# Performance work log

Hardware: AMD Instinct MI355X
Metric: run time of the kernel (lower is better)

The kernel has to match this reference:

```python
import math
import jax, jax.numpy as jnp
import numpy as np
from jax import lax

FEATURE_DIM = 1024
EMBED_DIM = 300
VOCAB = 32000
HIDDEN = 512
BATCH = 64
MAX_LEN = 40
S = 3  # number of feature maps summed in l_total


def setup_inputs() -> dict:
    key = jax.random.key(0)
    ks = jax.random.split(key, 10)
    l_total = jax.random.normal(ks[0], (S, BATCH, FEATURE_DIM), jnp.float32)
    encoded_captions = jax.random.randint(ks[1], (BATCH, MAX_LEN), 0, VOCAB)
    lengths = jax.random.randint(ks[2], (BATCH,), 5, MAX_LEN + 1)
    lengths = lengths.at[0].set(MAX_LEN)  # ensure max(decode_lengths) == MAX_LEN-1 (static)
    caption_lengths = lengths[:, None]
    # parameters (per PlainDecoder.init_weights / torch defaults)
    emb_weight = jax.random.uniform(ks[3], (VOCAB, EMBED_DIM), jnp.float32, -0.1, 0.1)
    k = 1.0 / math.sqrt(HIDDEN)
    W_ih = jax.random.uniform(ks[4], (4 * HIDDEN, EMBED_DIM + FEATURE_DIM), jnp.float32, -k, k)
    W_hh = jax.random.uniform(ks[5], (4 * HIDDEN, HIDDEN), jnp.float32, -k, k)
    b_ih = jax.random.uniform(ks[6], (4 * HIDDEN,), jnp.float32, -k, k)
    b_hh = jax.random.uniform(ks[7], (4 * HIDDEN,), jnp.float32, -k, k)
    wdc_W = jax.random.uniform(ks[8], (VOCAB, HIDDEN), jnp.float32, -0.1, 0.1)
    wdc_b = jnp.zeros((VOCAB,), jnp.float32)
    return {
        "l_total": l_total,
        "encoded_captions": encoded_captions,
        "caption_lengths": caption_lengths,
        "emb_weight": emb_weight,
        "W_ih": W_ih,
        "W_hh": W_hh,
        "b_ih": b_ih,
        "b_hh": b_hh,
        "wdc_W": wdc_W,
        "wdc_b": wdc_b,
    }


def reference(l_total, encoded_captions, caption_lengths, emb_weight, W_ih, W_hh, b_ih, b_hh, wdc_W, wdc_b):
    # l_total: (S, B, F) -> permute(1,2,0).sum(-1) -> (B, F)
    lt = jnp.transpose(l_total, (1, 2, 0)).sum(-1)
    lengths = caption_lengths[:, 0]
    sort_ind = jnp.argsort(-lengths)  # descending
    lengths_s = lengths[sort_ind]
    lt = lt[sort_ind]
    caps = encoded_captions[sort_ind]
    decode_lengths = lengths_s - 1
    embeds = emb_weight[caps]  # (B, L, E)

    T = caps.shape[1] - 1  # static max decode length (max length pinned in setup)
    B = caps.shape[0]
    H = W_hh.shape[1]

    emb_seq = jnp.transpose(embeds[:, :T, :], (1, 0, 2))  # (T, B, E)
    mask = jnp.arange(T)[:, None] < decode_lengths[None, :]  # (T, B)

    def step(carry, xs):
        h, c = carry
        emb_t, mask_t = xs
        x = jnp.concatenate([emb_t, lt], axis=1)  # (B, E+F)
        gates = x @ W_ih.T + h @ W_hh.T + b_ih + b_hh  # (B, 4H)
        i, f, g, o = jnp.split(gates, 4, axis=1)  # torch gate order: i,f,g,o
        i = jax.nn.sigmoid(i)
        f = jax.nn.sigmoid(f)
        g = jnp.tanh(g)
        o = jax.nn.sigmoid(o)
        c = f * c + i * g
        h = o * jnp.tanh(c)
        pred = h @ wdc_W.T + wdc_b  # (B, V)
        pred = jnp.where(mask_t[:, None], pred, jnp.zeros((), pred.dtype))
        return (h, c), pred

    h0 = jnp.zeros((B, H), lt.dtype)
    c0 = jnp.zeros((B, H), lt.dtype)
    _, preds = lax.scan(step, (h0, c0), (emb_seq, mask))  # (T, B, V)
    predictions = jnp.transpose(preds, (1, 0, 2))  # (B, T, V)
    return predictions, caps, decode_lengths, sort_ind
```

## Files before the change

### kernel.cpp

```cpp
#include <hip/hip_runtime.h>
#include <hip/hip_bf16.h>
#include <math.h>

typedef float f32x4 __attribute__((ext_vector_type(4)));
typedef __bf16 bf16x8 __attribute__((ext_vector_type(8)));
typedef __bf16 bf16x4 __attribute__((ext_vector_type(4)));
typedef unsigned long long u64;

#define BATCH   64
#define TSTEPS  39
#define HID     512
#define GATES   2048
#define NVOCAB  32000
#define EMBD    300
#define FEAT    1024
#define XDIM    1324

#define PRED_ELEMS (BATCH*TSTEPS*NVOCAB)

#define WS_CNT     0
#define WS_SORT    256
#define WS_DECLEN  512
#define WS_CAPS    1024
#define WS_BAR     16384
#define WS_LT      65536
#define WS_CONST   327680
#define WS_XP      1048576
#define WS_HALL    22020096
#define WS_WDCB    25165824

__device__ __forceinline__ u64 agent_load_u64(const u64* p) {
    return __hip_atomic_load(p, __ATOMIC_RELAXED, __HIP_MEMORY_SCOPE_AGENT);
}
__device__ __forceinline__ unsigned int agent_load_u32(const unsigned int* p) {
    return __hip_atomic_load(p, __ATOMIC_RELAXED, __HIP_MEMORY_SCOPE_AGENT);
}
__device__ __forceinline__ void agent_store_u32(unsigned int* p, unsigned int v) {
    __hip_atomic_store(p, v, __ATOMIC_RELAXED, __HIP_MEMORY_SCOPE_AGENT);
}

__global__ void k0_setup(const int* caplen, const int* enc,
                         float* out_caps, float* out_declen, float* out_sort,
                         int* ws_sort, int* ws_declen, int* ws_caps,
                         unsigned int* bar) {
    __shared__ int L[BATCH];
    __shared__ int sind[BATCH];
    int tid = threadIdx.x;
    for (int x = tid; x < 64*32; x += blockDim.x) bar[x] = 0u;
    if (tid < BATCH) L[tid] = caplen[tid];
    __syncthreads();
    if (tid < BATCH) {
        int len = L[tid];
        int rank = 0;
        for (int j = 0; j < BATCH; ++j) {
            int lj = L[j];
            if (lj > len || (lj == len && j < tid)) rank++;
        }
        sind[rank] = tid;
    }
    __syncthreads();
    if (tid < BATCH) {
        int src = sind[tid];
        ws_sort[tid] = src;
        int dl = L[src] - 1;
        ws_declen[tid] = dl;
        out_declen[tid] = (float)dl;
        out_sort[tid] = (float)src;
    }
    __syncthreads();
    for (int x = tid; x < BATCH*40; x += blockDim.x) {
        int b = x / 40, t = x % 40;
        int v = enc[sind[b]*40 + t];
        ws_caps[x] = v;
        out_caps[x] = (float)v;
    }
}

__global__ void k1_lt(const float* l_total, const int* ws_sort, float* lt) {
    int b = blockIdx.x;
    int ob = ws_sort[b];
    for (int k4 = threadIdx.x; k4 < FEAT/4; k4 += blockDim.x) {
        float4 a = ((const float4*)(l_total + (0*BATCH + ob)*FEAT))[k4];
        float4 c = ((const float4*)(l_total + (1*BATCH + ob)*FEAT))[k4];
        float4 d = ((const float4*)(l_total + (2*BATCH + ob)*FEAT))[k4];
        float4 r;
        r.x = a.x + c.x + d.x;  r.y = a.y + c.y + d.y;
        r.z = a.z + c.z + d.z;  r.w = a.w + c.w + d.w;
        ((float4*)(lt + b*FEAT))[k4] = r;
    }
}

__global__ void k2_const(const float* W_ih, const float* lt,
                         const float* b_ih, const float* b_hh, float* cst) {
    __shared__ float As[32][68];
    __shared__ float Bs[32][36];
    int ctile = blockIdx.x;
    int btile = blockIdx.y;
    int tid = threadIdx.x;
    int ty = tid >> 4, tx = tid & 15;
    float acc[4][2] = {};
    for (int kc = 0; kc < 32; ++kc) {
        __syncthreads();
        #pragma unroll
        for (int j = 0; j < 8; ++j) {
            int idx = tid + j*256;
            int c = idx >> 5, k = idx & 31;
            As[k][c] = W_ih[(ctile*64 + c)*XDIM + 300 + kc*32 + k];
        }
        #pragma unroll
        for (int j = 0; j < 4; ++j) {
            int idx = tid + j*256;
            int b = idx >> 5, k = idx & 31;
            Bs[k][b] = lt[(btile*32 + b)*FEAT + kc*32 + k];
        }
        __syncthreads();
        for (int k = 0; k < 32; ++k) {
            float4 av = *(const float4*)&As[k][ty*4];
            float2 bv = *(const float2*)&Bs[k][tx*2];
            acc[0][0] += av.x*bv.x; acc[0][1] += av.x*bv.y;
            acc[1][0] += av.y*bv.x; acc[1][1] += av.y*bv.y;
            acc[2][0] += av.z*bv.x; acc[2][1] += av.z*bv.y;
            acc[3][0] += av.w*bv.x; acc[3][1] += av.w*bv.y;
        }
    }
    #pragma unroll
    for (int i = 0; i < 4; ++i) {
        int cg = ctile*64 + ty*4 + i;
        float bias = b_ih[cg] + b_hh[cg];
        float2 o;
        o.x = acc[i][0] + bias; o.y = acc[i][1] + bias;
        *(float2*)&cst[cg*64 + btile*32 + tx*2] = o;
    }
}

__global__ void k3_xp(const float* W_ih, const float* emb, const int* ws_caps,
                      const float* cst, float* Xp) {
    __shared__ float As[20][68];
    __shared__ float Bs[20][68];
    int ctile = blockIdx.x;
    int t = blockIdx.y;
    int tid = threadIdx.x;
    int ty = tid >> 4, tx = tid & 15;
    float acc[4][4] = {};
    for (int kc = 0; kc < 15; ++kc) {
        __syncthreads();
        #pragma unroll
        for (int j = 0; j < 5; ++j) {
            int idx = tid + j*256;
            int c = idx / 20, k = idx % 20;
            As[k][c] = W_ih[(ctile*64 + c)*XDIM + kc*20 + k];
        }
        #pragma unroll
        for (int j = 0; j < 5; ++j) {
            int idx = tid + j*256;
            int b = idx / 20, k = idx % 20;
            int tok = ws_caps[b*40 + t];
            Bs[k][b] = emb[tok*EMBD + kc*20 + k];
        }
        __syncthreads();
        for (int k = 0; k < 20; ++k) {
            float4 av = *(const float4*)&As[k][ty*4];
            float4 bv = *(const float4*)&Bs[k][tx*4];
            acc[0][0] += av.x*bv.x; acc[0][1] += av.x*bv.y; acc[0][2] += av.x*bv.z; acc[0][3] += av.x*bv.w;
            acc[1][0] += av.y*bv.x; acc[1][1] += av.y*bv.y; acc[1][2] += av.y*bv.z; acc[1][3] += av.y*bv.w;
            acc[2][0] += av.z*bv.x; acc[2][1] += av.z*bv.y; acc[2][2] += av.z*bv.z; acc[2][3] += av.z*bv.w;
            acc[3][0] += av.w*bv.x; acc[3][1] += av.w*bv.y; acc[3][2] += av.w*bv.z; acc[3][3] += av.w*bv.w;
        }
    }
    #pragma unroll
    for (int i = 0; i < 4; ++i) {
        int cg = ctile*64 + ty*4 + i;
        float4 cs = *(const float4*)&cst[cg*64 + tx*4];
        float4 o;
        o.x = acc[i][0] + cs.x; o.y = acc[i][1] + cs.y;
        o.z = acc[i][2] + cs.z; o.w = acc[i][3] + cs.w;
        *(float4*)&Xp[(t*GATES + cg)*64 + tx*4] = o;
    }
}

__global__ void k4_cvt(const float* wdc, __bf16* wdcb) {
    int n4 = NVOCAB*HID/4;
    for (int i = blockIdx.x*blockDim.x + threadIdx.x; i < n4; i += gridDim.x*blockDim.x) {
        float4 v = ((const float4*)wdc)[i];
        bf16x4 o;
        o[0] = (__bf16)v.x; o[1] = (__bf16)v.y; o[2] = (__bf16)v.z; o[3] = (__bf16)v.w;
        ((bf16x4*)wdcb)[i] = o;
    }
}

__global__ void __launch_bounds__(256) k5_lstm(const float* W_hh, const float* Xp,
                                               __bf16* h_all, unsigned int* bar) {
    __shared__ float gates_lds[32][64];
    __shared__ float c_lds[8][64];
    __shared__ __bf16 h_s[64][8];
    int p = blockIdx.x;
    int tid = threadIdx.x;
    int l = tid & 63, w = tid >> 6;

    bf16x8 wfrag[2][16];
    #pragma unroll
    for (int mt = 0; mt < 2; ++mt) {
        int rr = mt*16 + (l & 15);
        int grow = (rr >> 3)*HID + p*8 + (rr & 7);
        const float* wrow = W_hh + grow*HID;
        #pragma unroll
        for (int kc = 0; kc < 16; ++kc) {
            int k0 = kc*32 + (l >> 4)*8;
            float4 f0 = *(const float4*)(wrow + k0);
            float4 f1 = *(const float4*)(wrow + k0 + 4);
            bf16x8 v;
            v[0]=(__bf16)f0.x; v[1]=(__bf16)f0.y; v[2]=(__bf16)f0.z; v[3]=(__bf16)f0.w;
            v[4]=(__bf16)f1.x; v[5]=(__bf16)f1.y; v[6]=(__bf16)f1.z; v[7]=(__bf16)f1.w;
            wfrag[mt][kc] = v;
        }
    }
    for (int x = tid; x < 8*64; x += 256) ((float*)c_lds)[x] = 0.0f;
    __syncthreads();

    int ulA = tid >> 6;
    int bA  = tid & 63;

    for (int t = 0; t < TSTEPS; ++t) {
        float xg[2][4];
        {
            const float* xpt = Xp + (size_t)t*GATES*64;
            int u0 = p*8 + ulA;
            #pragma unroll
            for (int g = 0; g < 4; ++g) {
                xg[0][g] = xpt[((size_t)g*512 + u0    )*64 + bA];
                xg[1][g] = xpt[((size_t)g*512 + u0 + 4)*64 + bA];
            }
        }

        if (t == 0) {
            for (int x = tid; x < 32*64; x += 256) ((float*)gates_lds)[x] = 0.0f;
        } else {
            f32x4 acc0 = {0.f,0.f,0.f,0.f};
            f32x4 acc1 = {0.f,0.f,0.f,0.f};
            int bb = w*16 + (l & 15);
            const u64* hq = (const u64*)(h_all + (size_t)(t-1)*BATCH*HID + bb*HID + (l >> 4)*8);
            u64 hl[16][2];
            #pragma unroll
            for (int kc = 0; kc < 16; ++kc) {
                hl[kc][0] = agent_load_u64(hq + kc*4);
                hl[kc][1] = agent_load_u64(hq + kc*4 + 1);
            }
            #pragma unroll
            for (int kc = 0; kc < 16; ++kc) {
                union { bf16x8 v; u64 u[2]; } uu;
                uu.u[0] = hl[kc][0]; uu.u[1] = hl[kc][1];
                acc0 = __builtin_amdgcn_mfma_f32_16x16x32_bf16(wfrag[0][kc], uu.v, acc0, 0, 0, 0);
                acc1 = __builtin_amdgcn_mfma_f32_16x16x32_bf16(wfrag[1][kc], uu.v, acc1, 0, 0, 0);
            }
            #pragma unroll
            for (int j = 0; j < 4; ++j) {
                gates_lds[(l>>4)*4 + j][bb]      = acc0[j];
                gates_lds[16 + (l>>4)*4 + j][bb] = acc1[j];
            }
        }
        __syncthreads();

        #pragma unroll
        for (int half = 0; half < 2; ++half) {
            int ul = ulA + half*4;
            int b  = bA;
            float gi = gates_lds[ul][b]      + xg[half][0];
            float gf = gates_lds[8+ul][b]    + xg[half][1];
            float gg = gates_lds[16+ul][b]   + xg[half][2];
            float go = gates_lds[24+ul][b]   + xg[half][3];
            float ig = 1.0f/(1.0f + expf(-gi));
            float fg = 1.0f/(1.0f + expf(-gf));
            float gv = tanhf(gg);
            float og = 1.0f/(1.0f + expf(-go));
            float c = fg * c_lds[ul][b] + ig * gv;
            c_lds[ul][b] = c;
            float h = og * tanhf(c);
            h_s[b][ul] = (__bf16)h;
        }
        __syncthreads();

        {
            int row = tid >> 2, seg = tid & 3;
            unsigned int val = ((const unsigned int*)&h_s[0][0])[row*4 + seg];
            unsigned int* dst = (unsigned int*)(h_all + ((size_t)t*BATCH + row)*HID + p*8);
            agent_store_u32(dst + seg, val);
        }

        if (t < TSTEPS - 1) {
            __syncthreads();
            unsigned int tgt = (unsigned int)(t + 1);
            if (tid == 0) agent_store_u32(bar + p*32, tgt);
            if (tid < 64) {
                while (agent_load_u32(bar + tid*32) < tgt)
                    __builtin_amdgcn_s_sleep(1);
            }
            __syncthreads();
        }
    }
}

__global__ void __launch_bounds__(256) k6_pred(const __bf16* h_all, const __bf16* wdcb,
                                               const float* wdc_b, const int* ws_declen,
                                               float* out) {
    __shared__ __bf16 As[128][40];
    __shared__ __bf16 Bs[128][40];
    int mtile = blockIdx.x;
    int ntile = blockIdx.y;
    int tid = threadIdx.x;
    int l = tid & 63, w = tid >> 6;
    int wm = w >> 1, wn = w & 1;

    f32x4 acc[4][4];
    #pragma unroll
    for (int i = 0; i < 4; ++i)
        #pragma unroll
        for (int j = 0; j < 4; ++j)
            acc[i][j] = (f32x4){0.f,0.f,0.f,0.f};

    for (int kc = 0; kc < 16; ++kc) {
        __syncthreads();
        #pragma unroll
        for (int j = 0; j < 2; ++j) {
            int idx = tid + j*256;
            int row = idx >> 2, seg = idx & 3;
            int rg = mtile*128 + row;
            bf16x8 v;
            if (rg < TSTEPS*BATCH) {
                v = *(const bf16x8*)(h_all + (size_t)rg*HID + kc*32 + seg*8);
            } else {
                #pragma unroll
                for (int q = 0; q < 8; ++q) v[q] = (__bf16)0.0f;
            }
            *(bf16x8*)&As[row][seg*8] = v;
            int cg = ntile*128 + row;
            *(bf16x8*)&Bs[row][seg*8] = *(const bf16x8*)(wdcb + (size_t)cg*HID + kc*32 + seg*8);
        }
        __syncthreads();
        bf16x8 af[4], bf[4];
        #pragma unroll
        for (int s = 0; s < 4; ++s) {
            af[s] = *(const bf16x8*)&As[wm*64 + s*16 + (l & 15)][(l >> 4)*8];
            bf[s] = *(const bf16x8*)&Bs[wn*64 + s*16 + (l & 15)][(l >> 4)*8];
        }
        #pragma unroll
        for (int sm = 0; sm < 4; ++sm)
            #pragma unroll
            for (int sn = 0; sn < 4; ++sn)
                acc[sm][sn] = __builtin_amdgcn_mfma_f32_16x16x32_bf16(af[sm], bf[sn], acc[sm][sn], 0, 0, 0);
    }

    #pragma unroll
    for (int sm = 0; sm < 4; ++sm) {
        #pragma unroll
        for (int j = 0; j < 4; ++j) {
            int R = mtile*128 + wm*64 + sm*16 + (l >> 4)*4 + j;
            if (R >= TSTEPS*BATCH) continue;
            int t = R >> 6, b = R & 63;
            int dl = ws_declen[b];
            #pragma unroll
            for (int sn = 0; sn < 4; ++sn) {
                int C = ntile*128 + wn*64 + sn*16 + (l & 15);
                float v = (t < dl) ? (acc[sm][sn][j] + wdc_b[C]) : 0.0f;
                out[((size_t)b*TSTEPS + t)*NVOCAB + C] = v;
            }
        }
    }
}

extern "C" void kernel_launch(void* const* d_in, const int* in_sizes, int n_in,
                              void* d_out, int out_size, void* d_ws, size_t ws_size,
                              hipStream_t stream) {
    const float* l_total = (const float*)d_in[0];
    const int*   enc     = (const int*)d_in[1];
    const int*   caplen  = (const int*)d_in[2];
    const float* emb     = (const float*)d_in[3];
    const float* W_ih    = (const float*)d_in[4];
    const float* W_hh    = (const float*)d_in[5];
    const float* b_ih    = (const float*)d_in[6];
    const float* b_hh    = (const float*)d_in[7];
    const float* wdc_W   = (const float*)d_in[8];
    const float* wdc_b   = (const float*)d_in[9];

    float* out = (float*)d_out;
    char* ws = (char*)d_ws;

    unsigned int* bar   = (unsigned int*)(ws + WS_BAR);
    int* ws_sort        = (int*)(ws + WS_SORT);
    int* ws_declen      = (int*)(ws + WS_DECLEN);
    int* ws_caps        = (int*)(ws + WS_CAPS);
    float* lt           = (float*)(ws + WS_LT);
    float* cst          = (float*)(ws + WS_CONST);
    float* Xp           = (float*)(ws + WS_XP);
    __bf16* h_all       = (__bf16*)(ws + WS_HALL);
    __bf16* wdcb        = (__bf16*)(ws + WS_WDCB);

    float* out_caps   = out + PRED_ELEMS;
    float* out_declen = out_caps + BATCH*40;
    float* out_sort   = out_declen + BATCH;

    k0_setup<<<1, 256, 0, stream>>>(caplen, enc, out_caps, out_declen, out_sort,
                                    ws_sort, ws_declen, ws_caps, bar);
    k1_lt<<<BATCH, 256, 0, stream>>>(l_total, ws_sort, lt);
    k2_const<<<dim3(32, 2), 256, 0, stream>>>(W_ih, lt, b_ih, b_hh, cst);
    k3_xp<<<dim3(32, TSTEPS), 256, 0, stream>>>(W_ih, emb, ws_caps, cst, Xp);
    k4_cvt<<<2048, 256, 0, stream>>>(wdc_W, wdcb);
    k5_lstm<<<64, 256, 0, stream>>>(W_hh, Xp, h_all, bar);
    k6_pred<<<dim3(20, NVOCAB/128), 256, 0, stream>>>(h_all, wdcb, wdc_b, ws_declen, out);
}
```

Measured before the change: 916.3 us.

## Fuse LSTM recurrence and vocab projection into one persistent kernel with step flags

Replaces the separate recurrence kernel and vocab-projection GEMM with one persistent 256-block kernel. The first 64 blocks run the LSTM recurrence at raised priority and publish a global step-done counter. All blocks pull projection tiles from an atomic work counter and spin until the hidden-state rows a tile needs are ready, so the GEMM and its large output writes overlap the serial recurrence. It also changes the h-load stride in the recurrent MFMA from kc*4 to kc*8. That appears to fix wrong h indexing in the old code, so results may change. The design relies on all blocks being co-resident and adds spin-wait overhead.

```diff
diff --git a/kernel.cpp b/kernel.cpp
--- a/kernel.cpp
+++ b/kernel.cpp
@@ -18,16 +18,23 @@
 
 #define PRED_ELEMS (BATCH*TSTEPS*NVOCAB)
 
-#define WS_CNT     0
-#define WS_SORT    256
-#define WS_DECLEN  512
-#define WS_CAPS    1024
-#define WS_BAR     16384
-#define WS_LT      65536
-#define WS_CONST   327680
-#define WS_XP      1048576
-#define WS_HALL    22020096
-#define WS_WDCB    25165824
+#define NT_M 20
+#define NT_N 250
+#define TOT_TILES (NT_M*NT_N)
+#define REC_BLOCKS 64
+#define GRID_BLOCKS 256
+
+#define WS_STEPDONE 0
+#define WS_TILECNT  128
+#define WS_SORT     256
+#define WS_DECLEN   512
+#define WS_CAPS     1024
+#define WS_BAR      16384
+#define WS_LT       65536
+#define WS_CONST    327680
+#define WS_XP       1048576
+#define WS_HALL     22020096
+#define WS_WDCB     25165824
 
 __device__ __forceinline__ u64 agent_load_u64(const u64* p) {
     return __hip_atomic_load(p, __ATOMIC_RELAXED, __HIP_MEMORY_SCOPE_AGENT);
@@ -42,10 +49,12 @@
 __global__ void k0_setup(const int* caplen, const int* enc,
                          float* out_caps, float* out_declen, float* out_sort,
                          int* ws_sort, int* ws_declen, int* ws_caps,
+                         unsigned int* step_done, unsigned int* tile_cnt,
                          unsigned int* bar) {
     __shared__ int L[BATCH];
     __shared__ int sind[BATCH];
     int tid = threadIdx.x;
+    if (tid == 0) { *step_done = 0u; *tile_cnt = 0u; }
     for (int x = tid; x < 64*32; x += blockDim.x) bar[x] = 0u;
     if (tid < BATCH) L[tid] = caplen[tid];
     __syncthreads();
@@ -188,181 +197,210 @@
     }
 }
 
-__global__ void __launch_bounds__(256) k5_lstm(const float* W_hh, const float* Xp,
-                                               __bf16* h_all, unsigned int* bar) {
-    __shared__ float gates_lds[32][64];
-    __shared__ float c_lds[8][64];
-    __shared__ __bf16 h_s[64][8];
-    int p = blockIdx.x;
+__global__ void __launch_bounds__(256) k5_fused(const float* W_hh, const float* Xp,
+                                                __bf16* h_all, unsigned int* bar,
+                                                unsigned int* step_done, unsigned int* tile_cnt,
+                                                const __bf16* wdcb, const float* wdc_b,
+                                                const int* ws_declen, float* out) {
+    __shared__ __align__(16) char lds_raw[20480];
+    __shared__ unsigned int tile_sh;
     int tid = threadIdx.x;
     int l = tid & 63, w = tid >> 6;
 
-    bf16x8 wfrag[2][16];
-    #pragma unroll
-    for (int mt = 0; mt < 2; ++mt) {
-        int rr = mt*16 + (l & 15);
-        int grow = (rr >> 3)*HID + p*8 + (rr & 7);
-        const float* wrow = W_hh + grow*HID;
+    if (blockIdx.x < REC_BLOCKS) {
+        float (*gates_lds)[64] = (float(*)[64])(lds_raw);
+        float (*c_lds)[64]     = (float(*)[64])(lds_raw + 8192);
+        __bf16 (*h_s)[8]       = (__bf16(*)[8])(lds_raw + 10240);
+        int p = blockIdx.x;
+
+        __builtin_amdgcn_s_setprio(1);
+
+        bf16x8 wfrag[2][16];
         #pragma unroll
-        for (int kc = 0; kc < 16; ++kc) {
-            int k0 = kc*32 + (l >> 4)*8;
-            float4 f0 = *(const float4*)(wrow + k0);
-            float4 f1 = *(const float4*)(wrow + k0 + 4);
-            bf16x8 v;
-            v[0]=(__bf16)f0.x; v[1]=(__bf16)f0.y; v[2]=(__bf16)f0.z; v[3]=(__bf16)f0.w;
-            v[4]=(__bf16)f1.x; v[5]=(__bf16)f1.y; v[6]=(__bf16)f1.z; v[7]=(__bf16)f1.w;
-            wfrag[mt][kc] = v;
-        }
-    }
-    for (int x = tid; x < 8*64; x += 256) ((float*)c_lds)[x] = 0.0f;
-    __syncthreads();
-
-    int ulA = tid >> 6;
-    int bA  = tid & 63;
-
-    for (int t = 0; t < TSTEPS; ++t) {
-        float xg[2][4];
-        {
-            const float* xpt = Xp + (size_t)t*GATES*64;
-            int u0 = p*8 + ulA;
-            #pragma unroll
-            for (int g = 0; g < 4; ++g) {
-                xg[0][g] = xpt[((size_t)g*512 + u0    )*64 + bA];
-                xg[1][g] = xpt[((size_t)g*512 + u0 + 4)*64 + bA];
-            }
-        }
-
-        if (t == 0) {
-            for (int x = tid; x < 32*64; x += 256) ((float*)gates_lds)[x] = 0.0f;
-        } else {
-            f32x4 acc0 = {0.f,0.f,0.f,0.f};
-            f32x4 acc1 = {0.f,0.f,0.f,0.f};
-            int bb = w*16 + (l & 15);
-            const u64* hq = (const u64*)(h_all + (size_t)(t-1)*BATCH*HID + bb*HID + (l >> 4)*8);
-            u64 hl[16][2];
+        for (int mt = 0; mt < 2; ++mt) {
+            int rr = mt*16 + (l & 15);
+            int grow = (rr >> 3)*HID + p*8 + (rr & 7);
+            const float* wrow = W_hh + grow*HID;
             #pragma unroll
             for (int kc = 0; kc < 16; ++kc) {
-                hl[kc][0] = agent_load_u64(hq + kc*4);
-                hl[kc][1] = agent_load_u64(hq + kc*4 + 1);
-            }
+                int k0 = kc*32 + (l >> 4)*8;
+                float4 f0 = *(const float4*)(wrow + k0);
+                float4 f1 = *(const float4*)(wrow + k0 + 4);
+                bf16x8 v;
+                v[0]=(__bf16)f0.x; v[1]=(__bf16)f0.y; v[2]=(__bf16)f0.z; v[3]=(__bf16)f0.w;
+                v[4]=(__bf16)f1.x; v[5]=(__bf16)f1.y; v[6]=(__bf16)f1.z; v[7]=(__bf16)f1.w;
+                wfrag[mt][kc] = v;
+            }
+        }
+        for (int x = tid; x < 8*64; x += 256) ((float*)c_lds)[x] = 0.0f;
+        __syncthreads();
+
+        int ulA = tid >> 6;
+        int bA  = tid & 63;
+
+        for (int t = 0; t < TSTEPS; ++t) {
+            float xg[2][4];
+            {
+                const float* xpt = Xp + (size_t)t*GATES*64;
+                int u0 = p*8 + ulA;
+                #pragma unroll
+                for (int g = 0; g < 4; ++g) {
+                    xg[0][g] = xpt[((size_t)g*512 + u0    )*64 + bA];
+                    xg[1][g] = xpt[((size_t)g*512 + u0 + 4)*64 + bA];
+                }
+            }
+
+            if (t == 0) {
+                for (int x = tid; x < 32*64; x += 256) ((float*)gates_lds)[x] = 0.0f;
+            } else {
+                int bb = w*16 + (l & 15);
+                const u64* hq = (const u64*)(h_all + (size_t)(t-1)*BATCH*HID + bb*HID + (l >> 4)*8);
+                u64 hl[16][2];
+                #pragma unroll
+                for (int kc = 0; kc < 16; ++kc) {
+                    hl[kc][0] = agent_load_u64(hq + kc*8);
+                    hl[kc][1] = agent_load_u64(hq + kc*8 + 1);
+                }
+                f32x4 acc0 = {0.f,0.f,0.f,0.f};
+                f32x4 acc1 = {0.f,0.f,0.f,0.f};
+                #pragma unroll
+                for (int kc = 0; kc < 16; ++kc) {
+                    union { bf16x8 v; u64 u[2]; } uu;
+                    uu.u[0] = hl[kc][0]; uu.u[1] = hl[kc][1];
+                    acc0 = __builtin_amdgcn_mfma_f32_16x16x32_bf16(wfrag[0][kc], uu.v, acc0, 0, 0, 0);
+                    acc1 = __builtin_amdgcn_mfma_f32_16x16x32_bf16(wfrag[1][kc], uu.v, acc1, 0, 0, 0);
+                }
+                #pragma unroll
+                for (int j = 0; j < 4; ++j) {
+                    gates_lds[(l>>4)*4 + j][bb]      = acc0[j];
+                    gates_lds[16 + (l>>4)*4 + j][bb] = acc1[j];
+                }
+            }
+            __syncthreads();
+
             #pragma unroll
-            for (int kc = 0; kc < 16; ++kc) {
-                union { bf16x8 v; u64 u[2]; } uu;
-                uu.u[0] = hl[kc][0]; uu.u[1] = hl[kc][1];
-                acc0 = __builtin_amdgcn_mfma_f32_16x16x32_bf16(wfrag[0][kc], uu.v, acc0, 0, 0, 0);
-                acc1 = __builtin_amdgcn_mfma_f32_16x16x32_bf16(wfrag[1][kc], uu.v, acc1, 0, 0, 0);
-            }
-            #pragma unroll
-            for (int j = 0; j < 4; ++j) {
-                gates_lds[(l>>4)*4 + j][bb]      = acc0[j];
-                gates_lds[16 + (l>>4)*4 + j][bb] = acc1[j];
-            }
-        }
-        __syncthreads();
-
-        #pragma unroll
-        for (int half = 0; half < 2; ++half) {
-            int ul = ulA + half*4;
-            int b  = bA;
-            float gi = gates_lds[ul][b]      + xg[half][0];
-            float gf = gates_lds[8+ul][b]    + xg[half][1];
-            float gg = gates_lds[16+ul][b]   + xg[half][2];
-            float go = gates_lds[24+ul][b]   + xg[half][3];
-            float ig = 1.0f/(1.0f + expf(-gi));
-            float fg = 1.0f/(1.0f + expf(-gf));
-            float gv = tanhf(gg);
-            float og = 1.0f/(1.0f + expf(-go));
-            float c = fg * c_lds[ul][b] + ig * gv;
-            c_lds[ul][b] = c;
-            float h = og * tanhf(c);
-            h_s[b][ul] = (__bf16)h;
-        }
-        __syncthreads();
-
-        {
-            int row = tid >> 2, seg = tid & 3;
-            unsigned int val = ((const unsigned int*)&h_s[0][0])[row*4 + seg];
-            unsigned int* dst = (unsigned int*)(h_all + ((size_t)t*BATCH + row)*HID + p*8);
-            agent_store_u32(dst + seg, val);
-        }
-
-        if (t < TSTEPS - 1) {
-            __syncthreads();
+            for (int half = 0; half < 2; ++half) {
+                int ul = ulA + half*4;
+                int b  = bA;
+                float gi = gates_lds[ul][b]      + xg[half][0];
+                float gf = gates_lds[8+ul][b]    + xg[half][1];
+                float gg = gates_lds[16+ul][b]   + xg[half][2];
+                float go = gates_lds[24+ul][b]   + xg[half][3];
+                float ig = 1.0f/(1.0f + expf(-gi));
+                float fg = 1.0f/(1.0f + expf(-gf));
+                float gv = tanhf(gg);
+                float og = 1.0f/(1.0f + expf(-go));
+                float c = fg * c_lds[ul][b] + ig * gv;
+                c_lds[ul][b] = c;
+                float h = og * tanhf(c);
+                h_s[b][ul] = (__bf16)h;
+            }
+            __syncthreads();
+
+            {
+                int row = tid >> 2, seg = tid & 3;
+                unsigned int val = ((const unsigned int*)&h_s[0][0])[row*4 + seg];
+                unsigned int* dst = (unsigned int*)(h_all + ((size_t)t*BATCH + row)*HID + p*8);
+                agent_store_u32(dst + seg, val);
+            }
+            __syncthreads();
+
             unsigned int tgt = (unsigned int)(t + 1);
             if (tid == 0) agent_store_u32(bar + p*32, tgt);
-            if (tid < 64) {
-                while (agent_load_u32(bar + tid*32) < tgt)
-                    __builtin_amdgcn_s_sleep(1);
-            }
-            __syncthreads();
-        }
-    }
-}
-
-__global__ void __launch_bounds__(256) k6_pred(const __bf16* h_all, const __bf16* wdcb,
-                                               const float* wdc_b, const int* ws_declen,
-                                               float* out) {
-    __shared__ __bf16 As[128][40];
-    __shared__ __bf16 Bs[128][40];
-    int mtile = blockIdx.x;
-    int ntile = blockIdx.y;
-    int tid = threadIdx.x;
-    int l = tid & 63, w = tid >> 6;
-    int wm = w >> 1, wn = w & 1;
-
-    f32x4 acc[4][4];
-    #pragma unroll
-    for (int i = 0; i < 4; ++i)
-        #pragma unroll
-        for (int j = 0; j < 4; ++j)
-            acc[i][j] = (f32x4){0.f,0.f,0.f,0.f};
-
-    for (int kc = 0; kc < 16; ++kc) {
-        __syncthreads();
-        #pragma unroll
-        for (int j = 0; j < 2; ++j) {
-            int idx = tid + j*256;
-            int row = idx >> 2, seg = idx & 3;
-            int rg = mtile*128 + row;
-            bf16x8 v;
-            if (rg < TSTEPS*BATCH) {
-                v = *(const bf16x8*)(h_all + (size_t)rg*HID + kc*32 + seg*8);
-            } else {
-                #pragma unroll
-                for (int q = 0; q < 8; ++q) v[q] = (__bf16)0.0f;
-            }
-            *(bf16x8*)&As[row][seg*8] = v;
-            int cg = ntile*128 + row;
-            *(bf16x8*)&Bs[row][seg*8] = *(const bf16x8*)(wdcb + (size_t)cg*HID + kc*32 + seg*8);
-        }
-        __syncthreads();
-        bf16x8 af[4], bf[4];
-        #pragma unroll
-        for (int s = 0; s < 4; ++s) {
-            af[s] = *(const bf16x8*)&As[wm*64 + s*16 + (l & 15)][(l >> 4)*8];
-            bf[s] = *(const bf16x8*)&Bs[wn*64 + s*16 + (l & 15)][(l >> 4)*8];
-        }
-        #pragma unroll
-        for (int sm = 0; sm < 4; ++sm)
+            if (t < TSTEPS - 1 || p == 0) {
+                if (tid < 64) {
+                    while (agent_load_u32(bar + tid*32) < tgt)
+                        __builtin_amdgcn_s_sleep(1);
+                    asm volatile("" ::: "memory");
+                    if (p == 0 && tid == 0) agent_store_u32(step_done, tgt);
+                }
+                __syncthreads();
+            }
+        }
+        __builtin_amdgcn_s_setprio(0);
+    }
+
+    {
+        __bf16 (*As)[40] = (__bf16(*)[40])(lds_raw);
+        __bf16 (*Bs)[40] = (__bf16(*)[40])(lds_raw + 10240);
+        int wm = (w >> 1), wn = (w & 1);
+
+        for (;;) {
+            if (tid == 0)
+                tile_sh = __hip_atomic_fetch_add(tile_cnt, 1u, __ATOMIC_RELAXED,
+                                                 __HIP_MEMORY_SCOPE_AGENT);
+            __syncthreads();
+            unsigned int tile = tile_sh;
+            __syncthreads();
+            if (tile >= TOT_TILES) break;
+            int mtile = tile / NT_N;
+            int ntile = tile % NT_N;
+            int thi = (mtile*128 + 127) >> 6;
+            if (thi > TSTEPS - 1) thi = TSTEPS - 1;
+            unsigned int need = (unsigned int)(thi + 1);
+            if (tid == 0) {
+                while (agent_load_u32(step_done) < need)
+                    __builtin_amdgcn_s_sleep(8);
+            }
+            __syncthreads();
+            asm volatile("" ::: "memory");
+
+            f32x4 acc[4][4];
             #pragma unroll
-            for (int sn = 0; sn < 4; ++sn)
-                acc[sm][sn] = __builtin_amdgcn_mfma_f32_16x16x32_bf16(af[sm], bf[sn], acc[sm][sn], 0, 0, 0);
-    }
-
-    #pragma unroll
-    for (int sm = 0; sm < 4; ++sm) {
-        #pragma unroll
-        for (int j = 0; j < 4; ++j) {
-            int R = mtile*128 + wm*64 + sm*16 + (l >> 4)*4 + j;
-            if (R >= TSTEPS*BATCH) continue;
-            int t = R >> 6, b = R & 63;
-            int dl = ws_declen[b];
+            for (int i = 0; i < 4; ++i)
+                #pragma unroll
+                for (int j = 0; j < 4; ++j)
+                    acc[i][j] = (f32x4){0.f,0.f,0.f,0.f};
+
+            for (int kc = 0; kc < 16; ++kc) {
+                __syncthreads();
+                #pragma unroll
+                for (int j = 0; j < 2; ++j) {
+                    int idx = tid + j*256;
+                    int row = idx >> 2, seg = idx & 3;
+                    int rg = mtile*128 + row;
+                    bf16x8 v;
+                    if (rg < TSTEPS*BATCH) {
+                        v = *(const bf16x8*)(h_all + (size_t)rg*HID + kc*32 + seg*8);
+                    } else {
+                        #pragma unroll
+                        for (int q = 0; q < 8; ++q) v[q] = (__bf16)0.0f;
+                    }
+                    *(bf16x8*)&As[row][seg*8] = v;
+                    int cg = ntile*128 + row;
+                    *(bf16x8*)&Bs[row][seg*8] = *(const bf16x8*)(wdcb + (size_t)cg*HID + kc*32 + seg*8);
+                }
+                __syncthreads();
+                bf16x8 af[4], bf[4];
+                #pragma unroll
+                for (int s = 0; s < 4; ++s) {
+                    af[s] = *(const bf16x8*)&As[wm*64 + s*16 + (l & 15)][(l >> 4)*8];
+                    bf[s] = *(const bf16x8*)&Bs[wn*64 + s*16 + (l & 15)][(l >> 4)*8];
+                }
+                #pragma unroll
+                for (int sm = 0; sm < 4; ++sm)
+                    #pragma unroll
+                    for (int sn = 0; sn < 4; ++sn)
+                        acc[sm][sn] = __builtin_amdgcn_mfma_f32_16x16x32_bf16(af[sm], bf[sn], acc[sm][sn], 0, 0, 0);
+            }
+
             #pragma unroll
-            for (int sn = 0; sn < 4; ++sn) {
-                int C = ntile*128 + wn*64 + sn*16 + (l & 15);
-                float v = (t < dl) ? (acc[sm][sn][j] + wdc_b[C]) : 0.0f;
-                out[((size_t)b*TSTEPS + t)*NVOCAB + C] = v;
-            }
+            for (int sm = 0; sm < 4; ++sm) {
+                #pragma unroll
+                for (int j = 0; j < 4; ++j) {
+                    int R = mtile*128 + wm*64 + sm*16 + (l >> 4)*4 + j;
+                    if (R >= TSTEPS*BATCH) continue;
+                    int t = R >> 6, b = R & 63;
+                    int dl = ws_declen[b];
+                    #pragma unroll
+                    for (int sn = 0; sn < 4; ++sn) {
+                        int C = ntile*128 + wn*64 + sn*16 + (l & 15);
+                        float v = (t < dl) ? (acc[sm][sn][j] + wdc_b[C]) : 0.0f;
+                        out[((size_t)b*TSTEPS + t)*NVOCAB + C] = v;
+                    }
+                }
+            }
+            __syncthreads();
         }
     }
 }
@@ -384,7 +422,9 @@
     float* out = (float*)d_out;
     char* ws = (char*)d_ws;
 
-    unsigned int* bar   = (unsigned int*)(ws + WS_BAR);
+    unsigned int* step_done = (unsigned int*)(ws + WS_STEPDONE);
+    unsigned int* tile_cnt  = (unsigned int*)(ws + WS_TILECNT);
+    unsigned int* bar       = (unsigned int*)(ws + WS_BAR);
     int* ws_sort        = (int*)(ws + WS_SORT);
     int* ws_declen      = (int*)(ws + WS_DECLEN);
     int* ws_caps        = (int*)(ws + WS_CAPS);
@@ -399,11 +439,13 @@
     float* out_sort   = out_declen + BATCH;
 
     k0_setup<<<1, 256, 0, stream>>>(caplen, enc, out_caps, out_declen, out_sort,
-                                    ws_sort, ws_declen, ws_caps, bar);
+                                    ws_sort, ws_declen, ws_caps,
+                                    step_done, tile_cnt, bar);
     k1_lt<<<BATCH, 256, 0, stream>>>(l_total, ws_sort, lt);
     k2_const<<<dim3(32, 2), 256, 0, stream>>>(W_ih, lt, b_ih, b_hh, cst);
     k3_xp<<<dim3(32, TSTEPS), 256, 0, stream>>>(W_ih, emb, ws_caps, cst, Xp);
     k4_cvt<<<2048, 256, 0, stream>>>(wdc_W, wdcb);
-    k5_lstm<<<64, 256, 0, stream>>>(W_hh, Xp, h_all, bar);
-    k6_pred<<<dim3(20, NVOCAB/128), 256, 0, stream>>>(h_all, wdcb, wdc_b, ws_declen, out);
-}
+    k5_fused<<<GRID_BLOCKS, 256, 0, stream>>>(W_hh, Xp, h_all, bar,
+                                              step_done, tile_cnt,
+                                              wdcb, wdc_b, ws_declen, out);
+}
```

New measurement: 940.0 us. +2.6%, slower.
